# Optimization experiments

Measured on AMD Instinct MI355X. Metric: run time of the kernel, lower is better.

## Reference

```python
import jax, jax.numpy as jnp
import numpy as np

GRID = 9          # grid_size -> output is GRID*GRID = 81 per pair
NB_VAR = 81
NB_FT = 2
HID = 256
NBLOCKS = 2
EPS = 1e-5

TI, TJ = np.triu_indices(NB_VAR, 1)  # 3240 pairs


def _bn(h, g, b):
    # BatchNorm1d in training mode: biased batch statistics over rows
    m = jnp.mean(h, axis=0)
    v = jnp.var(h, axis=0)
    return (h - m) * (g * jax.lax.rsqrt(v + EPS)) + b


def setup_inputs() -> dict:
    key = jax.random.key(0)
    ks = jax.random.split(key, 16)
    s_in = (2.0 / 4) ** 0.5
    s_h = (2.0 / HID) ** 0.5
    inp = {
        "x": jax.random.normal(ks[0], (4, NB_VAR, NB_FT), jnp.float32),
        "w_in": jax.random.normal(ks[1], (HID, 4), jnp.float32) * s_in,
        "b_in": jnp.zeros((HID,), jnp.float32),
        # per-ResBlock params stacked over leading NBLOCKS dim
        "g1": jnp.ones((NBLOCKS, HID), jnp.float32),
        "beta1": jnp.zeros((NBLOCKS, HID), jnp.float32),
        "w1": jax.random.normal(ks[2], (NBLOCKS, HID, HID), jnp.float32) * s_h,
        "bias1": jnp.zeros((NBLOCKS, HID), jnp.float32),
        "g2": jnp.ones((NBLOCKS, HID), jnp.float32),
        "beta2": jnp.zeros((NBLOCKS, HID), jnp.float32),
        "w2": jax.random.normal(ks[3], (NBLOCKS, HID, HID), jnp.float32) * s_h,
        "bias2": jnp.zeros((NBLOCKS, HID), jnp.float32),
        "fg": jnp.ones((HID,), jnp.float32),
        "fbeta": jnp.zeros((HID,), jnp.float32),
        "w_out": jax.random.normal(ks[4], (GRID * GRID, HID), jnp.float32) * s_h,
        "b_out": jnp.zeros((GRID * GRID,), jnp.float32),
    }
    return inp


def reference(x, w_in, b_in, g1, beta1, w1, bias1, g2, beta2, w2, bias2,
              fg, fbeta, w_out, b_out):
    bs, nb_var, nb_ft = x.shape
    # pairwise gather: concat features of each (i,j) pair, i<j -> (bs*P, 2*nb_ft)
    rr = jnp.concatenate([x[:, TI], x[:, TJ]], axis=-1).reshape(-1, 2 * nb_ft)

    h = jax.nn.relu(rr @ w_in.T + b_in)
    for k in range(NBLOCKS):
        z = jax.nn.relu(_bn(h, g1[k], beta1[k])) @ w1[k].T + bias1[k]
        z = jax.nn.relu(_bn(z, g2[k], beta2[k])) @ w2[k].T + bias2[k]
        h = h + z
    h = jax.nn.relu(_bn(h, fg, fbeta))
    pred = (h @ w_out.T + b_out).reshape(bs, -1, GRID, GRID)

    # symmetric scatter into (bs, V, V, G, G)
    out = jnp.zeros((bs, nb_var, nb_var, GRID, GRID), x.dtype)
    out = out.at[:, TI, TJ].set(pred)
    out = out.at[:, TJ, TI].set(jnp.swapaxes(pred, 2, 3))
    return out
```

## Files before the change

kernel.cpp:

```cpp
#include <hip/hip_runtime.h>

#define RTOT 12960
#define PAIRS 3240
#define NB_VAR 81
#define HID 256
#define EPS 1e-5f

#define BM 64
#define BN 64
#define LDB 264
#define NCPY 16

using bf8   = __attribute__((ext_vector_type(8))) short;
using f32x4 = __attribute__((ext_vector_type(4))) float;

__device__ inline ushort f2bf(float f) {
    union { float f; unsigned u; } c; c.f = f;
    unsigned u = c.u + 0x7fffu + ((c.u >> 16) & 1u);
    return (ushort)(u >> 16);
}
__device__ inline float bf2f(ushort h) {
    union { unsigned u; float f; } c; c.u = (unsigned)h << 16;
    return c.f;
}
__device__ inline unsigned pk2(float a, float b) {
    return (unsigned)f2bf(a) | ((unsigned)f2bf(b) << 16);
}
__device__ inline int2 pair_of(int p) {
    int i = (int)((161.0 - sqrt(25921.0 - 8.0 * (double)p)) * 0.5);
    if (i < 0) i = 0;
    while ((161 * (i + 1) - (i + 1) * (i + 1)) / 2 <= p) i++;
    while ((161 * i - i * i) / 2 > p) i--;
    int j = i + 1 + (p - (161 * i - i * i) / 2);
    return make_int2(i, j);
}

__device__ __forceinline__ void coeffs(const float* __restrict__ st,
                                       const float* __restrict__ g,
                                       const float* __restrict__ beta,
                                       float* sS, float* sT) {
    int tid = threadIdx.x;
    float s = 0.f, q = 0.f;
#pragma unroll
    for (int cp = 0; cp < NCPY; cp++) {
        s += st[cp * 512 + tid];
        q += st[cp * 512 + 256 + tid];
    }
    float m = s * (1.f / RTOT);
    float v = q * (1.f / RTOT) - m * m;
    float sc = g[tid] * rsqrtf(v + EPS);
    sS[tid] = sc;
    sT[tid] = fmaf(-m, sc, beta[tid]);
}

__device__ __forceinline__ bf8 ldA(const ushort* xr, int kst,
                                   const float* sS, const float* sT) {
    float4 s0 = *(const float4*)&sS[kst], s1 = *(const float4*)&sS[kst + 4];
    float4 t0 = *(const float4*)&sT[kst], t1 = *(const float4*)&sT[kst + 4];
    ushort xv[8];
    *(uint4*)xv = *(const uint4*)(xr + kst);
    unsigned pk[4];
    pk[0] = pk2(fmaxf(fmaf(bf2f(xv[0]), s0.x, t0.x), 0.f),
                fmaxf(fmaf(bf2f(xv[1]), s0.y, t0.y), 0.f));
    pk[1] = pk2(fmaxf(fmaf(bf2f(xv[2]), s0.z, t0.z), 0.f),
                fmaxf(fmaf(bf2f(xv[3]), s0.w, t0.w), 0.f));
    pk[2] = pk2(fmaxf(fmaf(bf2f(xv[4]), s1.x, t1.x), 0.f),
                fmaxf(fmaf(bf2f(xv[5]), s1.y, t1.y), 0.f));
    pk[3] = pk2(fmaxf(fmaf(bf2f(xv[6]), s1.z, t1.z), 0.f),
                fmaxf(fmaf(bf2f(xv[7]), s1.w, t1.w), 0.f));
    return *(bf8*)pk;
}

__global__ __launch_bounds__(256) void k_init(
        const float* __restrict__ x, const float* __restrict__ w_in,
        const float* __restrict__ b_in,
        const float* __restrict__ w1, const float* __restrict__ w2,
        const float* __restrict__ w_out, ushort* __restrict__ wbf,
        int2* __restrict__ pairs, float* __restrict__ out,
        ushort* __restrict__ h0, float* __restrict__ st) {
    __shared__ float feat[32][4];
    int tid = threadIdx.x;
    int gtid = blockIdx.x * 256 + tid;

    for (int i = gtid; i < 262144 + 81 * 256; i += 405 * 256) {
        float v;
        if (i < 131072)      v = w1[i];
        else if (i < 262144) v = w2[i - 131072];
        else                 v = w_out[i - 262144];
        wbf[i] = f2bf(v);
    }
    if (gtid < 4 * NB_VAR * 81) {
        int b = gtid / (NB_VAR * 81);
        int rem = gtid - b * (NB_VAR * 81);
        int i = rem / 81, t = rem - i * 81;
        out[((size_t)(b * NB_VAR + i) * NB_VAR + i) * 81 + t] = 0.f;
    }

    int r0 = blockIdx.x * 32;
    if (tid < 32) {
        int r = r0 + tid;
        int b = r / PAIRS, p = r - b * PAIRS;
        int2 ij = pair_of(p);
        if (r < PAIRS) pairs[r] = ij;
        const float* xb = x + b * NB_VAR * 2;
        feat[tid][0] = xb[ij.x * 2 + 0];
        feat[tid][1] = xb[ij.x * 2 + 1];
        feat[tid][2] = xb[ij.y * 2 + 0];
        feat[tid][3] = xb[ij.y * 2 + 1];
    }
    __syncthreads();
    float4 w = ((const float4*)w_in)[tid];
    float bi = b_in[tid];
    float s = 0.f, s2 = 0.f;
    for (int t = 0; t < 32; t++) {
        float v = fmaf(feat[t][0], w.x, fmaf(feat[t][1], w.y,
                  fmaf(feat[t][2], w.z, fmaf(feat[t][3], w.w, bi))));
        v = fmaxf(v, 0.f);
        h0[(size_t)(r0 + t) * HID + tid] = f2bf(v);
        s += v; s2 += v * v;
    }
    int cp = blockIdx.x & (NCPY - 1);
    atomicAdd(&st[cp * 512 + tid], s);
    atomicAdd(&st[cp * 512 + 256 + tid], s2);
}

__global__ __launch_bounds__(256) void k_gemm(
        const ushort* __restrict__ X, const float* __restrict__ stin,
        const float* __restrict__ g, const float* __restrict__ beta,
        const ushort* __restrict__ Wb, const float* __restrict__ bias,
        const ushort* __restrict__ res, ushort* __restrict__ Y,
        float* __restrict__ stout) {
    __shared__ ushort sB[BN * LDB];
    __shared__ float sS[HID], sT[HID];
    __shared__ float sCS[4][BN], sCQ[4][BN];

    int tid = threadIdx.x;
    coeffs(stin, g, beta, sS, sT);

    int id = blockIdx.x, bx, by;
    if (id < 800) { bx = (id >> 5) * 8 + (id & 7); by = (id >> 3) & 3; }
    else          { int j = id - 800; bx = 200 + (j >> 2); by = j & 3; }

    int bm0 = bx * BM;
    int bn0 = by * BN;
    {
        int row = tid >> 2, cq = tid & 3;
#pragma unroll
        for (int s = 0; s < 8; s++) {
            int col = cq * 8 + s * 32;
            uint4 wv = *(const uint4*)(Wb + (size_t)(bn0 + row) * HID + col);
            *(uint4*)&sB[row * LDB + col] = wv;
        }
    }
    __syncthreads();

    int lane = tid & 63, w = tid >> 6;
    int r16 = lane & 15, kq = lane >> 4;

    f32x4 acc[4] = {};
    int ar = min(bm0 + w * 16 + r16, RTOT - 1);
    const ushort* xr = X + (size_t)ar * HID;

#pragma unroll
    for (int kk = 0; kk < 8; kk++) {
        int kst = kk * 32 + kq * 8;
        bf8 af = ldA(xr, kst, sS, sT);
        bf8 b0 = *(const bf8*)&sB[(0 * 16 + r16) * LDB + kst];
        bf8 b1 = *(const bf8*)&sB[(1 * 16 + r16) * LDB + kst];
        bf8 b2 = *(const bf8*)&sB[(2 * 16 + r16) * LDB + kst];
        bf8 b3 = *(const bf8*)&sB[(3 * 16 + r16) * LDB + kst];
        acc[0] = __builtin_amdgcn_mfma_f32_16x16x32_bf16(af, b0, acc[0], 0, 0, 0);
        acc[1] = __builtin_amdgcn_mfma_f32_16x16x32_bf16(af, b1, acc[1], 0, 0, 0);
        acc[2] = __builtin_amdgcn_mfma_f32_16x16x32_bf16(af, b2, acc[2], 0, 0, 0);
        acc[3] = __builtin_amdgcn_mfma_f32_16x16x32_bf16(af, b3, acc[3], 0, 0, 0);
    }

    int rb = bm0 + w * 16;
#pragma unroll
    for (int n = 0; n < 4; n++) {
        int col = bn0 + n * 16 + r16;
        float bv = bias[col];
        float cs = 0.f, cq2 = 0.f;
#pragma unroll
        for (int i = 0; i < 4; i++) {
            int r = rb + kq * 4 + i;
            if (r < RTOT) {
                float v = acc[n][i] + bv;
                if (res) v += bf2f(res[(size_t)r * HID + col]);
                Y[(size_t)r * HID + col] = f2bf(v);
                cs += v; cq2 += v * v;
            }
        }
        cs += __shfl_xor(cs, 16); cq2 += __shfl_xor(cq2, 16);
        cs += __shfl_xor(cs, 32); cq2 += __shfl_xor(cq2, 32);
        if (lane < 16) {
            sCS[w][n * 16 + lane] = cs; sCQ[w][n * 16 + lane] = cq2;
        }
    }
    __syncthreads();
    if (tid < 2 * BN) {
        int col = tid & (BN - 1), q = tid >> 6;
        float v = q ? (sCQ[0][col] + sCQ[1][col] + sCQ[2][col] + sCQ[3][col])
                    : (sCS[0][col] + sCS[1][col] + sCS[2][col] + sCS[3][col]);
        int cp = id & (NCPY - 1);
        atomicAdd(&stout[cp * 512 + q * 256 + bn0 + col], v);
    }
}

__global__ __launch_bounds__(256) void k_gout(
        const ushort* __restrict__ X, const float* __restrict__ stin,
        const float* __restrict__ g, const float* __restrict__ beta,
        const ushort* __restrict__ Wb, const float* __restrict__ b_out,
        const int2* __restrict__ pairs, float* __restrict__ out) {
    __shared__ ushort sB[BN * LDB];
    __shared__ float sS[HID], sT[HID];

    int tid = threadIdx.x;
    coeffs(stin, g, beta, sS, sT);

    int id = blockIdx.x, bx, by;
    if (id < 400) { bx = (id >> 4) * 8 + (id & 7); by = (id >> 3) & 1; }
    else          { int j = id - 400; bx = 200 + (j >> 1); by = j & 1; }

    int bm0 = bx * BM;
    int bn0 = by * BN;
    {
        int row = tid >> 2, cq = tid & 3;
        int gn = bn0 + row; gn = gn < 81 ? gn : 80;
#pragma unroll
        for (int s = 0; s < 8; s++) {
            int col = cq * 8 + s * 32;
            uint4 wv = *(const uint4*)(Wb + (size_t)gn * HID + col);
            *(uint4*)&sB[row * LDB + col] = wv;
        }
    }
    __syncthreads();

    int lane = tid & 63, w = tid >> 6;
    int r16 = lane & 15, kq = lane >> 4;

    f32x4 acc[4] = {};
    int ar = min(bm0 + w * 16 + r16, RTOT - 1);
    const ushort* xr = X + (size_t)ar * HID;

#pragma unroll
    for (int kk = 0; kk < 8; kk++) {
        int kst = kk * 32 + kq * 8;
        bf8 af = ldA(xr, kst, sS, sT);
        bf8 b0 = *(const bf8*)&sB[(0 * 16 + r16) * LDB + kst];
        bf8 b1 = *(const bf8*)&sB[(1 * 16 + r16) * LDB + kst];
        bf8 b2 = *(const bf8*)&sB[(2 * 16 + r16) * LDB + kst];
        bf8 b3 = *(const bf8*)&sB[(3 * 16 + r16) * LDB + kst];
        acc[0] = __builtin_amdgcn_mfma_f32_16x16x32_bf16(af, b0, acc[0], 0, 0, 0);
        acc[1] = __builtin_amdgcn_mfma_f32_16x16x32_bf16(af, b1, acc[1], 0, 0, 0);
        acc[2] = __builtin_amdgcn_mfma_f32_16x16x32_bf16(af, b2, acc[2], 0, 0, 0);
        acc[3] = __builtin_amdgcn_mfma_f32_16x16x32_bf16(af, b3, acc[3], 0, 0, 0);
    }

    int rb = bm0 + w * 16;
#pragma unroll
    for (int n = 0; n < 4; n++) {
        int t = bn0 + n * 16 + r16;
        if (t >= 81) continue;
        int gi = t / 9, gj = t - gi * 9;
        int ttr = gj * 9 + gi;
        float bb = b_out[t];
#pragma unroll
        for (int i = 0; i < 4; i++) {
            int r = rb + kq * 4 + i;
            if (r >= RTOT) continue;
            int b = r / PAIRS, p = r - b * PAIRS;
            int2 ij = pairs[p];
            size_t base1 = ((size_t)(b * NB_VAR + ij.x) * NB_VAR + ij.y) * 81;
            size_t base2 = ((size_t)(b * NB_VAR + ij.y) * NB_VAR + ij.x) * 81;
            float v = acc[n][i] + bb;
            out[base1 + t] = v;
            out[base2 + ttr] = v;
        }
    }
}

extern "C" void kernel_launch(void* const* d_in, const int* in_sizes, int n_in,
                              void* d_out, int out_size, void* d_ws, size_t ws_size,
                              hipStream_t stream) {
    const float* x     = (const float*)d_in[0];
    const float* w_in  = (const float*)d_in[1];
    const float* b_in  = (const float*)d_in[2];
    const float* g1    = (const float*)d_in[3];
    const float* beta1 = (const float*)d_in[4];
    const float* w1    = (const float*)d_in[5];
    const float* bias1 = (const float*)d_in[6];
    const float* g2    = (const float*)d_in[7];
    const float* beta2 = (const float*)d_in[8];
    const float* w2    = (const float*)d_in[9];
    const float* bias2 = (const float*)d_in[10];
    const float* fg    = (const float*)d_in[11];
    const float* fbeta = (const float*)d_in[12];
    const float* w_out = (const float*)d_in[13];
    const float* b_out = (const float*)d_in[14];
    float* out = (float*)d_out;

    ushort* buf0 = (ushort*)d_ws;
    ushort* buf1 = buf0 + (size_t)RTOT * HID;
    ushort* buf2 = buf1 + (size_t)RTOT * HID;
    ushort* wbf  = buf2 + (size_t)RTOT * HID;
    float* stats = (float*)(wbf + 5 * 65536);
    int2*  pairs = (int2*)(stats + 5 * NCPY * 512);

    hipMemsetAsync(stats, 0, 5 * NCPY * 512 * sizeof(float), stream);
    k_init<<<405, 256, 0, stream>>>(x, w_in, b_in, w1, w2, w_out, wbf,
                                    pairs, out, buf0, stats + 0 * NCPY * 512);

    k_gemm<<<812, 256, 0, stream>>>(buf0, stats + 0 * NCPY * 512, g1, beta1,
                                    wbf + 0 * 65536, bias1, nullptr, buf1, stats + 1 * NCPY * 512);
    k_gemm<<<812, 256, 0, stream>>>(buf1, stats + 1 * NCPY * 512, g2, beta2,
                                    wbf + 2 * 65536, bias2, buf0, buf2, stats + 2 * NCPY * 512);
    k_gemm<<<812, 256, 0, stream>>>(buf2, stats + 2 * NCPY * 512, g1 + HID, beta1 + HID,
                                    wbf + 1 * 65536, bias1 + HID, nullptr, buf1, stats + 3 * NCPY * 512);
    k_gemm<<<812, 256, 0, stream>>>(buf1, stats + 3 * NCPY * 512, g2 + HID, beta2 + HID,
                                    wbf + 3 * 65536, bias2 + HID, buf2, buf0, stats + 4 * NCPY * 512);
    k_gout<<<406, 256, 0, stream>>>(buf0, stats + 4 * NCPY * 512, fg, fbeta,
                                    wbf + 4 * 65536, b_out, pairs, out);
}
```

Baseline: 82.23 us.

## Prepack weights into MFMA fragment layout and read B directly from global

```diff
diff --git a/kernel.cpp b/kernel.cpp
--- a/kernel.cpp
+++ b/kernel.cpp
@@ -8,7 +8,6 @@
 
 #define BM 64
 #define BN 64
-#define LDB 264
 #define NCPY 16
 
 using bf8   = __attribute__((ext_vector_type(8))) short;
@@ -75,19 +74,36 @@
         const float* __restrict__ x, const float* __restrict__ w_in,
         const float* __restrict__ b_in,
         const float* __restrict__ w1, const float* __restrict__ w2,
-        const float* __restrict__ w_out, ushort* __restrict__ wbf,
+        const float* __restrict__ w_out, ushort* __restrict__ pw,
         int2* __restrict__ pairs, float* __restrict__ out,
         ushort* __restrict__ h0, float* __restrict__ st) {
     __shared__ float feat[32][4];
     int tid = threadIdx.x;
     int gtid = blockIdx.x * 256 + tid;
 
-    for (int i = gtid; i < 262144 + 81 * 256; i += 405 * 256) {
-        float v;
-        if (i < 131072)      v = w1[i];
-        else if (i < 262144) v = w2[i - 131072];
-        else                 v = w_out[i - 262144];
-        wbf[i] = f2bf(v);
+    for (int i = gtid; i < 262144 + 24576; i += 405 * 256) {
+        ushort val;
+        if (i < 262144) {
+            int L = i >> 16, r = i & 65535;
+            int cg = r >> 14, r2 = r & 16383;
+            int kk = r2 >> 11, r3 = r2 & 2047;
+            int n = r3 >> 9, r4 = r3 & 511;
+            int lane = r4 >> 3, e = r4 & 7;
+            int col = cg * 64 + n * 16 + (lane & 15);
+            int k = kk * 32 + (lane >> 4) * 8 + e;
+            const float* Ws = (L == 0) ? w1 : (L == 1) ? w2
+                           : (L == 2) ? w1 + 65536 : w2 + 65536;
+            val = f2bf(Ws[col * HID + k]);
+        } else {
+            int j = i - 262144;
+            int f = j >> 12, r2 = j & 4095;
+            int kk = r2 >> 9, r3 = r2 & 511;
+            int lane = r3 >> 3, e = r3 & 7;
+            int col = f * 16 + (lane & 15);
+            int k = kk * 32 + (lane >> 4) * 8 + e;
+            val = (col < 81) ? f2bf(w_out[col * HID + k]) : (ushort)0;
+        }
+        pw[i] = val;
     }
     if (gtid < 4 * NB_VAR * 81) {
         int b = gtid / (NB_VAR * 81);
@@ -124,34 +140,23 @@
     atomicAdd(&st[cp * 512 + 256 + tid], s2);
 }
 
-__global__ __launch_bounds__(256) void k_gemm(
+__global__ __launch_bounds__(256, 4) void k_gemm(
         const ushort* __restrict__ X, const float* __restrict__ stin,
         const float* __restrict__ g, const float* __restrict__ beta,
-        const ushort* __restrict__ Wb, const float* __restrict__ bias,
+        const ushort* __restrict__ PW, const float* __restrict__ bias,
         const ushort* __restrict__ res, ushort* __restrict__ Y,
         float* __restrict__ stout) {
-    __shared__ ushort sB[BN * LDB];
     __shared__ float sS[HID], sT[HID];
     __shared__ float sCS[4][BN], sCQ[4][BN];
 
     int tid = threadIdx.x;
-    coeffs(stin, g, beta, sS, sT);
-
     int id = blockIdx.x, bx, by;
     if (id < 800) { bx = (id >> 5) * 8 + (id & 7); by = (id >> 3) & 3; }
     else          { int j = id - 800; bx = 200 + (j >> 2); by = j & 3; }
-
     int bm0 = bx * BM;
     int bn0 = by * BN;
-    {
-        int row = tid >> 2, cq = tid & 3;
-#pragma unroll
-        for (int s = 0; s < 8; s++) {
-            int col = cq * 8 + s * 32;
-            uint4 wv = *(const uint4*)(Wb + (size_t)(bn0 + row) * HID + col);
-            *(uint4*)&sB[row * LDB + col] = wv;
-        }
-    }
+
+    coeffs(stin, g, beta, sS, sT);
     __syncthreads();
 
     int lane = tid & 63, w = tid >> 6;
@@ -160,15 +165,17 @@
     f32x4 acc[4] = {};
     int ar = min(bm0 + w * 16 + r16, RTOT - 1);
     const ushort* xr = X + (size_t)ar * HID;
+    const ushort* pb = PW + ((size_t)by << 14) + lane * 8;
 
 #pragma unroll
     for (int kk = 0; kk < 8; kk++) {
         int kst = kk * 32 + kq * 8;
         bf8 af = ldA(xr, kst, sS, sT);
-        bf8 b0 = *(const bf8*)&sB[(0 * 16 + r16) * LDB + kst];
-        bf8 b1 = *(const bf8*)&sB[(1 * 16 + r16) * LDB + kst];
-        bf8 b2 = *(const bf8*)&sB[(2 * 16 + r16) * LDB + kst];
-        bf8 b3 = *(const bf8*)&sB[(3 * 16 + r16) * LDB + kst];
+        const ushort* pk = pb + (kk << 11);
+        bf8 b0 = *(const bf8*)(pk + 0 * 512);
+        bf8 b1 = *(const bf8*)(pk + 1 * 512);
+        bf8 b2 = *(const bf8*)(pk + 2 * 512);
+        bf8 b3 = *(const bf8*)(pk + 3 * 512);
         acc[0] = __builtin_amdgcn_mfma_f32_16x16x32_bf16(af, b0, acc[0], 0, 0, 0);
         acc[1] = __builtin_amdgcn_mfma_f32_16x16x32_bf16(af, b1, acc[1], 0, 0, 0);
         acc[2] = __builtin_amdgcn_mfma_f32_16x16x32_bf16(af, b2, acc[2], 0, 0, 0);
@@ -207,33 +214,21 @@
     }
 }
 
-__global__ __launch_bounds__(256) void k_gout(
+__global__ __launch_bounds__(256, 4) void k_gout(
         const ushort* __restrict__ X, const float* __restrict__ stin,
         const float* __restrict__ g, const float* __restrict__ beta,
-        const ushort* __restrict__ Wb, const float* __restrict__ b_out,
+        const ushort* __restrict__ PWo, const float* __restrict__ b_out,
         const int2* __restrict__ pairs, float* __restrict__ out) {
-    __shared__ ushort sB[BN * LDB];
     __shared__ float sS[HID], sT[HID];
 
     int tid = threadIdx.x;
-    coeffs(stin, g, beta, sS, sT);
-
     int id = blockIdx.x, bx, by;
     if (id < 400) { bx = (id >> 4) * 8 + (id & 7); by = (id >> 3) & 1; }
     else          { int j = id - 400; bx = 200 + (j >> 1); by = j & 1; }
-
     int bm0 = bx * BM;
     int bn0 = by * BN;
-    {
-        int row = tid >> 2, cq = tid & 3;
-        int gn = bn0 + row; gn = gn < 81 ? gn : 80;
-#pragma unroll
-        for (int s = 0; s < 8; s++) {
-            int col = cq * 8 + s * 32;
-            uint4 wv = *(const uint4*)(Wb + (size_t)gn * HID + col);
-            *(uint4*)&sB[row * LDB + col] = wv;
-        }
-    }
+
+    coeffs(stin, g, beta, sS, sT);
     __syncthreads();
 
     int lane = tid & 63, w = tid >> 6;
@@ -247,14 +242,13 @@
     for (int kk = 0; kk < 8; kk++) {
         int kst = kk * 32 + kq * 8;
         bf8 af = ldA(xr, kst, sS, sT);
-        bf8 b0 = *(const bf8*)&sB[(0 * 16 + r16) * LDB + kst];
-        bf8 b1 = *(const bf8*)&sB[(1 * 16 + r16) * LDB + kst];
-        bf8 b2 = *(const bf8*)&sB[(2 * 16 + r16) * LDB + kst];
-        bf8 b3 = *(const bf8*)&sB[(3 * 16 + r16) * LDB + kst];
-        acc[0] = __builtin_amdgcn_mfma_f32_16x16x32_bf16(af, b0, acc[0], 0, 0, 0);
-        acc[1] = __builtin_amdgcn_mfma_f32_16x16x32_bf16(af, b1, acc[1], 0, 0, 0);
-        acc[2] = __builtin_amdgcn_mfma_f32_16x16x32_bf16(af, b2, acc[2], 0, 0, 0);
-        acc[3] = __builtin_amdgcn_mfma_f32_16x16x32_bf16(af, b3, acc[3], 0, 0, 0);
+#pragma unroll
+        for (int n = 0; n < 4; n++) {
+            int f = by * 4 + n;
+            if (f >= 6) continue;
+            bf8 bv = *(const bf8*)(PWo + ((f * 8 + kk) << 9) + lane * 8);
+            acc[n] = __builtin_amdgcn_mfma_f32_16x16x32_bf16(af, bv, acc[n], 0, 0, 0);
+        }
     }
 
     int rb = bm0 + w * 16;
@@ -303,22 +297,22 @@
     ushort* buf0 = (ushort*)d_ws;
     ushort* buf1 = buf0 + (size_t)RTOT * HID;
     ushort* buf2 = buf1 + (size_t)RTOT * HID;
-    ushort* wbf  = buf2 + (size_t)RTOT * HID;
-    float* stats = (float*)(wbf + 5 * 65536);
+    ushort* pw   = buf2 + (size_t)RTOT * HID;
+    float* stats = (float*)(pw + 262144 + 24576);
     int2*  pairs = (int2*)(stats + 5 * NCPY * 512);
 
     hipMemsetAsync(stats, 0, 5 * NCPY * 512 * sizeof(float), stream);
-    k_init<<<405, 256, 0, stream>>>(x, w_in, b_in, w1, w2, w_out, wbf,
+    k_init<<<405, 256, 0, stream>>>(x, w_in, b_in, w1, w2, w_out, pw,
                                     pairs, out, buf0, stats + 0 * NCPY * 512);
 
     k_gemm<<<812, 256, 0, stream>>>(buf0, stats + 0 * NCPY * 512, g1, beta1,
-                                    wbf + 0 * 65536, bias1, nullptr, buf1, stats + 1 * NCPY * 512);
+                                    pw + 0 * 65536, bias1, nullptr, buf1, stats + 1 * NCPY * 512);
     k_gemm<<<812, 256, 0, stream>>>(buf1, stats + 1 * NCPY * 512, g2, beta2,
-                                    wbf + 2 * 65536, bias2, buf0, buf2, stats + 2 * NCPY * 512);
+                                    pw + 1 * 65536, bias2, buf0, buf2, stats + 2 * NCPY * 512);
     k_gemm<<<812, 256, 0, stream>>>(buf2, stats + 2 * NCPY * 512, g1 + HID, beta1 + HID,
-                                    wbf + 1 * 65536, bias1 + HID, nullptr, buf1, stats + 3 * NCPY * 512);
+                                    pw + 2 * 65536, bias1 + HID, nullptr, buf1, stats + 3 * NCPY * 512);
     k_gemm<<<812, 256, 0, stream>>>(buf1, stats + 3 * NCPY * 512, g2 + HID, beta2 + HID,
-                                    wbf + 3 * 65536, bias2 + HID, buf2, buf0, stats + 4 * NCPY * 512);
+                                    pw + 3 * 65536, bias2 + HID, buf2, buf0, stats + 4 * NCPY * 512);
     k_gout<<<406, 256, 0, stream>>>(buf0, stats + 4 * NCPY * 512, fg, fbeta,
-                                    wbf + 4 * 65536, b_out, pairs, out);
-}
+                                    pw + 4 * 65536, b_out, pairs, out);
+}
```

New measurement: 91.35 us. +11.1%, slower.

## Fold stats zeroing into init kernel and replace atomics with per-block partials

Applied to the files above, without the earlier changes.

```diff
diff --git a/kernel.cpp b/kernel.cpp
--- a/kernel.cpp
+++ b/kernel.cpp
@@ -10,6 +10,10 @@
 #define BN 64
 #define LDB 264
 #define NCPY 16
+#define IBLK 40
+#define IROWS 324
+#define S0SZ (IBLK * 512)
+#define SLSZ (NCPY * 512)
 
 using bf8   = __attribute__((ext_vector_type(8))) short;
 using f32x4 = __attribute__((ext_vector_type(4))) float;
@@ -35,14 +39,13 @@
     return make_int2(i, j);
 }
 
-__device__ __forceinline__ void coeffs(const float* __restrict__ st,
+__device__ __forceinline__ void coeffs(const float* __restrict__ st, int ncpy,
                                        const float* __restrict__ g,
                                        const float* __restrict__ beta,
                                        float* sS, float* sT) {
     int tid = threadIdx.x;
     float s = 0.f, q = 0.f;
-#pragma unroll
-    for (int cp = 0; cp < NCPY; cp++) {
+    for (int cp = 0; cp < ncpy; cp++) {
         s += st[cp * 512 + tid];
         q += st[cp * 512 + 256 + tid];
     }
@@ -71,61 +74,69 @@
     return *(bf8*)pk;
 }
 
-__global__ __launch_bounds__(256) void k_init(
+__global__ __launch_bounds__(512) void k_init(
         const float* __restrict__ x, const float* __restrict__ w_in,
         const float* __restrict__ b_in,
         const float* __restrict__ w1, const float* __restrict__ w2,
         const float* __restrict__ w_out, ushort* __restrict__ wbf,
         int2* __restrict__ pairs, float* __restrict__ out,
-        ushort* __restrict__ h0, float* __restrict__ st) {
-    __shared__ float feat[32][4];
+        ushort* __restrict__ h0, float* __restrict__ stats) {
+    __shared__ float feat[IROWS][4];
+    __shared__ float part[2][2][256];
     int tid = threadIdx.x;
-    int gtid = blockIdx.x * 256 + tid;
-
-    for (int i = gtid; i < 262144 + 81 * 256; i += 405 * 256) {
+    int b = blockIdx.x;
+    int gtid = b * 512 + tid;
+
+    for (int i = gtid; i < 262144 + 81 * 256; i += IBLK * 512) {
         float v;
         if (i < 131072)      v = w1[i];
         else if (i < 262144) v = w2[i - 131072];
         else                 v = w_out[i - 262144];
         wbf[i] = f2bf(v);
     }
-    if (gtid < 4 * NB_VAR * 81) {
-        int b = gtid / (NB_VAR * 81);
-        int rem = gtid - b * (NB_VAR * 81);
-        int i = rem / 81, t = rem - i * 81;
-        out[((size_t)(b * NB_VAR + i) * NB_VAR + i) * 81 + t] = 0.f;
-    }
-
-    int r0 = blockIdx.x * 32;
-    if (tid < 32) {
-        int r = r0 + tid;
-        int b = r / PAIRS, p = r - b * PAIRS;
+    for (int i = gtid; i < 4 * NB_VAR * 81; i += IBLK * 512) {
+        int bb = i / (NB_VAR * 81);
+        int rem = i - bb * (NB_VAR * 81);
+        int ii = rem / 81, t = rem - ii * 81;
+        out[((size_t)(bb * NB_VAR + ii) * NB_VAR + ii) * 81 + t] = 0.f;
+    }
+    for (int i = gtid; i < 4 * SLSZ; i += IBLK * 512)
+        stats[S0SZ + i] = 0.f;
+
+    if (tid < IROWS) {
+        int r = b * IROWS + tid;
+        int bb = r / PAIRS, p = r - bb * PAIRS;
         int2 ij = pair_of(p);
         if (r < PAIRS) pairs[r] = ij;
-        const float* xb = x + b * NB_VAR * 2;
+        const float* xb = x + bb * NB_VAR * 2;
         feat[tid][0] = xb[ij.x * 2 + 0];
         feat[tid][1] = xb[ij.x * 2 + 1];
         feat[tid][2] = xb[ij.y * 2 + 0];
         feat[tid][3] = xb[ij.y * 2 + 1];
     }
     __syncthreads();
-    float4 w = ((const float4*)w_in)[tid];
-    float bi = b_in[tid];
+
+    int col = tid & 255, sub = tid >> 8;
+    float4 w = ((const float4*)w_in)[col];
+    float bi = b_in[col];
     float s = 0.f, s2 = 0.f;
-    for (int t = 0; t < 32; t++) {
-        float v = fmaf(feat[t][0], w.x, fmaf(feat[t][1], w.y,
-                  fmaf(feat[t][2], w.z, fmaf(feat[t][3], w.w, bi))));
+    int rl0 = sub * 162;
+    for (int t = 0; t < 162; t++) {
+        int rl = rl0 + t;
+        float v = fmaf(feat[rl][0], w.x, fmaf(feat[rl][1], w.y,
+                  fmaf(feat[rl][2], w.z, fmaf(feat[rl][3], w.w, bi))));
         v = fmaxf(v, 0.f);
-        h0[(size_t)(r0 + t) * HID + tid] = f2bf(v);
+        h0[(size_t)(b * IROWS + rl) * HID + col] = f2bf(v);
         s += v; s2 += v * v;
     }
-    int cp = blockIdx.x & (NCPY - 1);
-    atomicAdd(&st[cp * 512 + tid], s);
-    atomicAdd(&st[cp * 512 + 256 + tid], s2);
+    part[sub][0][col] = s;
+    part[sub][1][col] = s2;
+    __syncthreads();
+    stats[b * 512 + sub * 256 + col] = part[0][sub][col] + part[1][sub][col];
 }
 
 __global__ __launch_bounds__(256) void k_gemm(
-        const ushort* __restrict__ X, const float* __restrict__ stin,
+        const ushort* __restrict__ X, const float* __restrict__ stin, int ncpyIn,
         const float* __restrict__ g, const float* __restrict__ beta,
         const ushort* __restrict__ Wb, const float* __restrict__ bias,
         const ushort* __restrict__ res, ushort* __restrict__ Y,
@@ -135,7 +146,7 @@
     __shared__ float sCS[4][BN], sCQ[4][BN];
 
     int tid = threadIdx.x;
-    coeffs(stin, g, beta, sS, sT);
+    coeffs(stin, ncpyIn, g, beta, sS, sT);
 
     int id = blockIdx.x, bx, by;
     if (id < 800) { bx = (id >> 5) * 8 + (id & 7); by = (id >> 3) & 3; }
@@ -216,7 +227,7 @@
     __shared__ float sS[HID], sT[HID];
 
     int tid = threadIdx.x;
-    coeffs(stin, g, beta, sS, sT);
+    coeffs(stin, NCPY, g, beta, sS, sT);
 
     int id = blockIdx.x, bx, by;
     if (id < 400) { bx = (id >> 4) * 8 + (id & 7); by = (id >> 3) & 1; }
@@ -305,20 +316,25 @@
     ushort* buf2 = buf1 + (size_t)RTOT * HID;
     ushort* wbf  = buf2 + (size_t)RTOT * HID;
     float* stats = (float*)(wbf + 5 * 65536);
-    int2*  pairs = (int2*)(stats + 5 * NCPY * 512);
-
-    hipMemsetAsync(stats, 0, 5 * NCPY * 512 * sizeof(float), stream);
-    k_init<<<405, 256, 0, stream>>>(x, w_in, b_in, w1, w2, w_out, wbf,
-                                    pairs, out, buf0, stats + 0 * NCPY * 512);
-
-    k_gemm<<<812, 256, 0, stream>>>(buf0, stats + 0 * NCPY * 512, g1, beta1,
-                                    wbf + 0 * 65536, bias1, nullptr, buf1, stats + 1 * NCPY * 512);
-    k_gemm<<<812, 256, 0, stream>>>(buf1, stats + 1 * NCPY * 512, g2, beta2,
-                                    wbf + 2 * 65536, bias2, buf0, buf2, stats + 2 * NCPY * 512);
-    k_gemm<<<812, 256, 0, stream>>>(buf2, stats + 2 * NCPY * 512, g1 + HID, beta1 + HID,
-                                    wbf + 1 * 65536, bias1 + HID, nullptr, buf1, stats + 3 * NCPY * 512);
-    k_gemm<<<812, 256, 0, stream>>>(buf1, stats + 3 * NCPY * 512, g2 + HID, beta2 + HID,
-                                    wbf + 3 * 65536, bias2 + HID, buf2, buf0, stats + 4 * NCPY * 512);
-    k_gout<<<406, 256, 0, stream>>>(buf0, stats + 4 * NCPY * 512, fg, fbeta,
+    int2*  pairs = (int2*)(stats + S0SZ + 4 * SLSZ);
+
+    float* S0 = stats;
+    float* S1 = stats + S0SZ;
+    float* S2 = S1 + SLSZ;
+    float* S3 = S2 + SLSZ;
+    float* S4 = S3 + SLSZ;
+
+    k_init<<<IBLK, 512, 0, stream>>>(x, w_in, b_in, w1, w2, w_out, wbf,
+                                     pairs, out, buf0, stats);
+
+    k_gemm<<<812, 256, 0, stream>>>(buf0, S0, IBLK, g1, beta1,
+                                    wbf + 0 * 65536, bias1, nullptr, buf1, S1);
+    k_gemm<<<812, 256, 0, stream>>>(buf1, S1, NCPY, g2, beta2,
+                                    wbf + 2 * 65536, bias2, buf0, buf2, S2);
+    k_gemm<<<812, 256, 0, stream>>>(buf2, S2, NCPY, g1 + HID, beta1 + HID,
+                                    wbf + 1 * 65536, bias1 + HID, nullptr, buf1, S3);
+    k_gemm<<<812, 256, 0, stream>>>(buf1, S3, NCPY, g2 + HID, beta2 + HID,
+                                    wbf + 3 * 65536, bias2 + HID, buf2, buf0, S4);
+    k_gout<<<406, 256, 0, stream>>>(buf0, S4, fg, fbeta,
                                     wbf + 4 * 65536, b_out, pairs, out);
 }
```

Result: slower. 104.3 us (+26.9%).
